# Optimization experiments

Measured on AMD Instinct MI355X. Metric: run time of the kernel, lower is better.

The kernel has to match this reference:

```python
import jax, jax.numpy as jnp
import numpy as np


def _sobel_weights():
    # ImageGradientsLayer: fixed Sobel x/y filters, shape (O=2, I=1, 3, 3)
    gx = jnp.array([[-1., 0., 1.], [-2., 0., 2.], [-1., 0., 1.]], dtype=jnp.float32)
    gy = jnp.array([[-1., -2., -1.], [0., 0., 0.], [1., 2., 1.]], dtype=jnp.float32)
    return jnp.stack([gx, gy])[:, None, :, :]


def _orientation_weights():
    # SIFTOrientationLayer: 8 unit orientation vectors + 2x2 identity, shape (10, 2)
    ratios = jnp.arange(0.125, 2.125, 0.25, dtype=jnp.float32)  # 8 values
    ang = ratios * jnp.pi
    vec = jnp.stack([jnp.cos(ang), jnp.sin(ang)], axis=1)  # (8, 2)
    return jnp.concatenate([vec, jnp.eye(2, dtype=jnp.float32)], axis=0)  # (10, 2)


def setup_inputs() -> dict:
    key = jax.random.key(0)
    x = jax.random.normal(key, (8, 1, 1024, 1024), dtype=jnp.float32)
    return {"x": x, "sobel_w": _sobel_weights(), "orient_w": _orientation_weights()}


def reference(x, sobel_w, orient_w):
    # 1) ImageGradientsLayer: 3x3 Sobel conv, padding=1 -> (B, 2, H, W)
    grads = jax.lax.conv_general_dilated(
        x, sobel_w, window_strides=(1, 1), padding=((1, 1), (1, 1)),
        dimension_numbers=("NCHW", "OIHW", "NCHW"))
    # 2) SIFTOrientationLayer: 1x1 conv == channel projection -> (B, 10, H, W)
    proj = jnp.einsum("bchw,oc->bohw", grads, orient_w)
    # 3) HistogramLayer: one-hot(argmax of orientation dots) * gradient magnitude
    cosines = proj[:, :8]          # (B, 8, H, W)
    im_grads = proj[:, 8:]         # (B, 2, H, W) == grads (identity rows)
    magnitudes = jnp.sqrt(jnp.sum(im_grads * im_grads, axis=1))  # (B, H, W)
    max_idx = jnp.argmax(cosines, axis=1)                        # (B, H, W)
    onehot = jax.nn.one_hot(max_idx, 8, axis=1, dtype=x.dtype)   # (B, 8, H, W)
    hist = onehot * magnitudes[:, None, :, :]
    # 4) SubGridAccumulationLayer: depthwise 4x4 all-ones conv, pad 2 -> (B, 8, H+1, W+1)
    ones_k = jnp.ones((8, 1, 4, 4), dtype=x.dtype)
    out = jax.lax.conv_general_dilated(
        hist, ones_k, window_strides=(1, 1), padding=((2, 2), (2, 2)),
        dimension_numbers=("NCHW", "OIHW", "NCHW"), feature_group_count=8)
    return out
```

## Files before the change

kernel.cpp:

```cpp
#include <hip/hip_runtime.h>
#include <math.h>


#define TWC 61
#define WTH 16
#define WPB 4
#define BTH (WPB*WTH)
#define XC 66
#define XR (BTH+5)
#define PLANE 1050625
#define NCT 17
#define NRT 17

__device__ __forceinline__ float wshl1(float v) {
    return __int_as_float(
        __builtin_amdgcn_update_dpp(0, __float_as_int(v), 0x130, 0xf, 0xf, true));
}

__global__ __launch_bounds__(256, 4)
void sift_fused(const float* __restrict__ x,
                const float* __restrict__ ow,
                float* __restrict__ out)
{
    __shared__ float sx[XR * XC];

    const int tid  = threadIdx.x;
    const int lane = tid & 63;
    const int wv   = tid >> 6;

    const int flat = blockIdx.x + NCT * (blockIdx.y + NRT * blockIdx.z);
    const int bb = flat & 7;
    const int t  = flat >> 3;
    const int bx = t % NCT;
    const int by = t / NCT;
    const int j0 = bx * TWC;
    const int r0 = by * BTH;

    const float* xb = x + (size_t)bb * 1024 * 1024;
    for (int p = tid; p < XR * XC; p += 256) {
        int r = p / XC, c = p - r * XC;
        int gr = r0 - 3 + r, gc = j0 - 3 + c;
        float v = 0.0f;
        if ((unsigned)gr < 1024u && (unsigned)gc < 1024u)
            v = xb[(size_t)gr * 1024 + gc];
        sx[p] = v;
    }
    __syncthreads();

    const int rbase = r0 + WTH * wv;
    if (rbase > 1024) return;

    float wcn[8], wsn[8];
    #pragma unroll
    for (int o = 0; o < 8; ++o) { wcn[o] = ow[2*o]; wsn[o] = ow[2*o+1]; }

    const int gcol = j0 - 2 + lane;
    const bool colok = (unsigned)gcol < 1024u;
    const int gj = j0 + lane;
    const bool canstore = (lane < TWC) && (gj <= 1024);

    float* po[8];
    #pragma unroll
    for (int o = 0; o < 8; ++o) po[o] = out + (size_t)(bb * 8 + o) * PLANE;

    const float* px = sx + (WTH * wv) * XC + lane;
    int hrow = rbase - 2;
    int orow = rbase;
    int vo   = rbase * 1025 + gj;

    float dd0, dd1, dd2, dd3, ww0, ww1, ww2, ww3;
    float cA[8], cB[8], PP0[8], PP1[8], PP2[8], PP3[8];

#define XROWLOAD(DD, WW) { \
    float n0 = px[0], n1 = px[1], n2 = px[2]; px += XC; \
    DD = n2 - n0; \
    WW = n0 + 2.0f*n1 + n2; \
}

#define HSTEP(DT, DM, DB, WT, WB, CP, CC, PR, PC, DOP, DOFIN) { \
    XROWLOAD(DB, WB) \
    float gx = DT + 2.0f*DM + DB; \
    float gy = WB - WT; \
    float msq = gx*gx + gy*gy; \
    float m = (colok && (unsigned)hrow < 1024u) \
                ? __builtin_amdgcn_sqrtf(msq) : 0.0f; \
    hrow++; \
    float pj0 = gx*wcn[0] + gy*wsn[0]; \
    float pj1 = gx*wcn[1] + gy*wsn[1]; \
    float pj2 = gx*wcn[2] + gy*wsn[2]; \
    float pj3 = gx*wcn[3] + gy*wsn[3]; \
    float pj4 = gx*wcn[4] + gy*wsn[4]; \
    float pj5 = gx*wcn[5] + gy*wsn[5]; \
    float pj6 = gx*wcn[6] + gy*wsn[6]; \
    float pj7 = gx*wcn[7] + gy*wsn[7]; \
    bool g01 = pj1 > pj0; float b01 = g01 ? pj1 : pj0; int i01 = g01 ? 1 : 0; \
    bool g23 = pj3 > pj2; float b23 = g23 ? pj3 : pj2; int i23 = g23 ? 3 : 2; \
    bool g45 = pj5 > pj4; float b45 = g45 ? pj5 : pj4; int i45 = g45 ? 5 : 4; \
    bool g67 = pj7 > pj6; float b67 = g67 ? pj7 : pj6; int i67 = g67 ? 7 : 6; \
    bool gA = b23 > b01; float bA = gA ? b23 : b01; int iA = gA ? i23 : i01; \
    bool gB = b67 > b45; float bB = gB ? b67 : b45; int iB = gB ? i67 : i45; \
    int idx = (bB > bA) ? iB : iA; \
    _Pragma("unroll") \
    for (int o = 0; o < 8; ++o) CC[o] = (idx == o) ? m : 0.0f; \
    if (DOP) { \
        _Pragma("unroll") \
        for (int o = 0; o < 8; ++o) PC[o] = CP[o] + CC[o]; \
    } \
    if (DOFIN) { \
        bool ok = canstore && (orow <= 1024); \
        _Pragma("unroll") \
        for (int o = 0; o < 8; ++o) { \
            float v = PR[o] + PC[o]; \
            v += wshl1(v);                  \
            v += wshl1(wshl1(v));           \
            if (ok) po[o][vo] = v; \
        } \
        vo += 1025; orow++; \
    } \
}

    XROWLOAD(dd0, ww0)
    XROWLOAD(dd1, ww1)
    HSTEP(dd0, dd1, dd2, ww0, ww2, cA, cB, PP0, PP0, 0, 0)
    HSTEP(dd1, dd2, dd3, ww1, ww3, cB, cA, PP0, PP1, 1, 0)
    HSTEP(dd2, dd3, dd0, ww2, ww0, cA, cB, PP0, PP2, 1, 0)

    #pragma unroll 1
    for (int it = 0; it < 4; ++it) {
        HSTEP(dd3, dd0, dd1, ww3, ww1, cB, cA, PP1, PP3, 1, 1)
        HSTEP(dd0, dd1, dd2, ww0, ww2, cA, cB, PP2, PP0, 1, 1)
        HSTEP(dd1, dd2, dd3, ww1, ww3, cB, cA, PP3, PP1, 1, 1)
        HSTEP(dd2, dd3, dd0, ww2, ww0, cA, cB, PP0, PP2, 1, 1)
    }

#undef HSTEP
#undef XROWLOAD
}

extern "C" void kernel_launch(void* const* d_in, const int* in_sizes, int n_in,
                              void* d_out, int out_size, void* d_ws, size_t ws_size,
                              hipStream_t stream)
{
    (void)in_sizes; (void)n_in; (void)d_ws; (void)ws_size; (void)out_size;
    const float* x  = (const float*)d_in[0];
    const float* ow = (const float*)d_in[2];
    float* out = (float*)d_out;

    dim3 grid(NCT, NRT, 8);
    sift_fused<<<grid, 256, 0, stream>>>(x, ow, out);
}
```

Baseline: 88.49 us.

## Drop LDS staging; load rows directly with float2, two columns per lane

Replaces the shared-memory tile load and block barrier with per-lane direct global float2 loads of each input row, prefetched one row ahead in registers. Each lane now computes two output columns, using DPP lane shifts for the horizontal neighbours. Blocks become 9-wave column strips over 33-row bands. This is meant to remove LDS traffic, the sync, and halo overhead per output, at the cost of higher register pressure and unaligned or redundant global loads.

```diff
diff --git a/kernel.cpp b/kernel.cpp
--- a/kernel.cpp
+++ b/kernel.cpp
@@ -2,139 +2,165 @@
 #include <math.h>
 
 
-#define TWC 61
-#define WTH 16
-#define WPB 4
-#define BTH (WPB*WTH)
-#define XC 66
-#define XR (BTH+5)
+#define BROWS 33
+#define NBANDS 32
+#define STRIPW 124
 #define PLANE 1050625
-#define NCT 17
-#define NRT 17
 
 __device__ __forceinline__ float wshl1(float v) {
     return __int_as_float(
         __builtin_amdgcn_update_dpp(0, __float_as_int(v), 0x130, 0xf, 0xf, true));
 }
 
-__global__ __launch_bounds__(256, 4)
+__global__ __launch_bounds__(576, 3)
 void sift_fused(const float* __restrict__ x,
                 const float* __restrict__ ow,
                 float* __restrict__ out)
 {
-    __shared__ float sx[XR * XC];
-
     const int tid  = threadIdx.x;
     const int lane = tid & 63;
     const int wv   = tid >> 6;
 
-    const int flat = blockIdx.x + NCT * (blockIdx.y + NRT * blockIdx.z);
-    const int bb = flat & 7;
-    const int t  = flat >> 3;
-    const int bx = t % NCT;
-    const int by = t / NCT;
-    const int j0 = bx * TWC;
-    const int r0 = by * BTH;
+    const int flat = blockIdx.x + NBANDS * blockIdx.y;
+    const int bb   = flat & 7;
+    const int band = flat >> 3;
+    const int r0 = band * BROWS;
+    const int j0 = wv * STRIPW;
 
     const float* xb = x + (size_t)bb * 1024 * 1024;
-    for (int p = tid; p < XR * XC; p += 256) {
-        int r = p / XC, c = p - r * XC;
-        int gr = r0 - 3 + r, gc = j0 - 3 + c;
-        float v = 0.0f;
-        if ((unsigned)gr < 1024u && (unsigned)gc < 1024u)
-            v = xb[(size_t)gr * 1024 + gc];
-        sx[p] = v;
-    }
-    __syncthreads();
-
-    const int rbase = r0 + WTH * wv;
-    if (rbase > 1024) return;
 
     float wcn[8], wsn[8];
     #pragma unroll
     for (int o = 0; o < 8; ++o) { wcn[o] = ow[2*o]; wsn[o] = ow[2*o+1]; }
 
-    const int gcol = j0 - 2 + lane;
-    const bool colok = (unsigned)gcol < 1024u;
-    const int gj = j0 + lane;
-    const bool canstore = (lane < TWC) && (gj <= 1024);
+    const int c1 = j0 - 4 + 2*lane;
+    const int s1 = min(max(c1,     0), 1022);
+    const int s2 = min(max(c1 + 2, 0), 1022);
+    const float mB = ((unsigned)(c1+1) < 1024u) ? 1.f : 0.f;
+    const float mC = ((unsigned)(c1+2) < 1024u) ? 1.f : 0.f;
+    const float mD = ((unsigned)(c1+3) < 1024u) ? 1.f : 0.f;
+
+    const int h0 = j0 - 2 + 2*lane;
+    const float cm0 = ((unsigned)h0     < 1024u) ? 1.f : 0.f;
+    const float cm1 = ((unsigned)(h0+1) < 1024u) ? 1.f : 0.f;
+
+    const int oc0 = j0 + 2*lane;
+    const bool st0 = (2*lane   < STRIPW) && (oc0   <= 1024);
+    const bool st1 = (2*lane+1 < STRIPW) && (oc0+1 <= 1024);
 
     float* po[8];
     #pragma unroll
-    for (int o = 0; o < 8; ++o) po[o] = out + (size_t)(bb * 8 + o) * PLANE;
+    for (int o = 0; o < 8; ++o) po[o] = out + (size_t)(bb*8 + o) * PLANE;
 
-    const float* px = sx + (WTH * wv) * XC + lane;
-    int hrow = rbase - 2;
-    int orow = rbase;
-    int vo   = rbase * 1025 + gj;
+    int vo   = r0 * 1025 + oc0;
+    int orow = r0;
+    int gr   = r0 - 3;
+    int hrow = r0 - 2;
 
-    float dd0, dd1, dd2, dd3, ww0, ww1, ww2, ww3;
-    float cA[8], cB[8], PP0[8], PP1[8], PP2[8], PP3[8];
+    float RD[4][2], RW[4][2];
+    float CEXP[2][2][8];
+    float PP[4][2][8];
+    float2 pv1, pv2;
 
-#define XROWLOAD(DD, WW) { \
-    float n0 = px[0], n1 = px[1], n2 = px[2]; px += XC; \
-    DD = n2 - n0; \
-    WW = n0 + 2.0f*n1 + n2; \
+#define XISSUE() { \
+    if ((unsigned)gr < 1024u) { \
+        const float* rp = xb + ((size_t)(unsigned)gr << 10); \
+        pv1 = *reinterpret_cast<const float2*>(rp + s1); \
+        pv2 = *reinterpret_cast<const float2*>(rp + s2); \
+    } else { pv1.x = 0.f; pv1.y = 0.f; pv2.x = 0.f; pv2.y = 0.f; } \
+    gr++; \
 }
 
-#define HSTEP(DT, DM, DB, WT, WB, CP, CC, PR, PC, DOP, DOFIN) { \
-    XROWLOAD(DB, WB) \
-    float gx = DT + 2.0f*DM + DB; \
-    float gy = WB - WT; \
-    float msq = gx*gx + gy*gy; \
-    float m = (colok && (unsigned)hrow < 1024u) \
-                ? __builtin_amdgcn_sqrtf(msq) : 0.0f; \
-    hrow++; \
-    float pj0 = gx*wcn[0] + gy*wsn[0]; \
-    float pj1 = gx*wcn[1] + gy*wsn[1]; \
-    float pj2 = gx*wcn[2] + gy*wsn[2]; \
-    float pj3 = gx*wcn[3] + gy*wsn[3]; \
-    float pj4 = gx*wcn[4] + gy*wsn[4]; \
-    float pj5 = gx*wcn[5] + gy*wsn[5]; \
-    float pj6 = gx*wcn[6] + gy*wsn[6]; \
-    float pj7 = gx*wcn[7] + gy*wsn[7]; \
+#define XCOMMIT(SB) { \
+    float B_ = pv1.y * mB, C_ = pv2.x * mC, D_ = pv2.y * mD; \
+    float E_ = wshl1(C_); \
+    RD[SB][0] = D_ - B_; \
+    RD[SB][1] = E_ - C_; \
+    RW[SB][0] = B_ + 2.0f*C_ + D_; \
+    RW[SB][1] = C_ + 2.0f*D_ + E_; \
+}
+
+#define TOURN8(RES, GX, GY) { \
+    float pj0 = (GX)*wcn[0] + (GY)*wsn[0]; \
+    float pj1 = (GX)*wcn[1] + (GY)*wsn[1]; \
+    float pj2 = (GX)*wcn[2] + (GY)*wsn[2]; \
+    float pj3 = (GX)*wcn[3] + (GY)*wsn[3]; \
+    float pj4 = (GX)*wcn[4] + (GY)*wsn[4]; \
+    float pj5 = (GX)*wcn[5] + (GY)*wsn[5]; \
+    float pj6 = (GX)*wcn[6] + (GY)*wsn[6]; \
+    float pj7 = (GX)*wcn[7] + (GY)*wsn[7]; \
     bool g01 = pj1 > pj0; float b01 = g01 ? pj1 : pj0; int i01 = g01 ? 1 : 0; \
     bool g23 = pj3 > pj2; float b23 = g23 ? pj3 : pj2; int i23 = g23 ? 3 : 2; \
     bool g45 = pj5 > pj4; float b45 = g45 ? pj5 : pj4; int i45 = g45 ? 5 : 4; \
     bool g67 = pj7 > pj6; float b67 = g67 ? pj7 : pj6; int i67 = g67 ? 7 : 6; \
     bool gA = b23 > b01; float bA = gA ? b23 : b01; int iA = gA ? i23 : i01; \
     bool gB = b67 > b45; float bB = gB ? b67 : b45; int iB = gB ? i67 : i45; \
-    int idx = (bB > bA) ? iB : iA; \
+    RES = (bB > bA) ? iB : iA; \
+}
+
+#define HSTEP(ST, SM, SB, EC, EP, PW, PRD, DOP, DOFIN) { \
+    XCOMMIT(SB) \
+    XISSUE() \
+    float rowm = ((unsigned)hrow < 1024u) ? 1.f : 0.f; \
+    hrow++; \
     _Pragma("unroll") \
-    for (int o = 0; o < 8; ++o) CC[o] = (idx == o) ? m : 0.0f; \
+    for (int c_ = 0; c_ < 2; ++c_) { \
+        float gx = RD[ST][c_] + 2.0f*RD[SM][c_] + RD[SB][c_]; \
+        float gy = RW[SB][c_] - RW[ST][c_]; \
+        float m = __builtin_amdgcn_sqrtf(gx*gx + gy*gy) \
+                    * (rowm * (c_ ? cm1 : cm0)); \
+        int idx_; \
+        TOURN8(idx_, gx, gy) \
+        _Pragma("unroll") \
+        for (int o = 0; o < 8; ++o) \
+            CEXP[EC][c_][o] = (idx_ == o) ? m : 0.0f; \
+    } \
     if (DOP) { \
         _Pragma("unroll") \
-        for (int o = 0; o < 8; ++o) PC[o] = CP[o] + CC[o]; \
+        for (int c_ = 0; c_ < 2; ++c_) { \
+            _Pragma("unroll") \
+            for (int o = 0; o < 8; ++o) \
+                PP[PW][c_][o] = CEXP[EP][c_][o] + CEXP[EC][c_][o]; \
+        } \
     } \
     if (DOFIN) { \
-        bool ok = canstore && (orow <= 1024); \
+        bool rowok = (orow <= 1024); \
         _Pragma("unroll") \
         for (int o = 0; o < 8; ++o) { \
-            float v = PR[o] + PC[o]; \
-            v += wshl1(v);                  \
-            v += wshl1(wshl1(v));           \
-            if (ok) po[o][vo] = v; \
+            float A  = PP[PRD][0][o] + PP[PW][0][o]; \
+            float Bv = PP[PRD][1][o] + PP[PW][1][o]; \
+            float S  = A + Bv; \
+            float Sd = wshl1(S); \
+            float Ad2 = wshl1(wshl1(A)); \
+            float Ev = S + Sd; \
+            float Ov = Bv + Sd + Ad2; \
+            if (rowok && st0) po[o][vo]   = Ev; \
+            if (rowok && st1) po[o][vo+1] = Ov; \
         } \
         vo += 1025; orow++; \
     } \
 }
 
-    XROWLOAD(dd0, ww0)
-    XROWLOAD(dd1, ww1)
-    HSTEP(dd0, dd1, dd2, ww0, ww2, cA, cB, PP0, PP0, 0, 0)
-    HSTEP(dd1, dd2, dd3, ww1, ww3, cB, cA, PP0, PP1, 1, 0)
-    HSTEP(dd2, dd3, dd0, ww2, ww0, cA, cB, PP0, PP2, 1, 0)
+    XISSUE()
+    XCOMMIT(0) XISSUE()
+    XCOMMIT(1) XISSUE()
+    HSTEP(0,1,2, 0,1, 0,0, 0, 0)
+    HSTEP(1,2,3, 1,0, 1,3, 1, 0)
+    HSTEP(2,3,0, 0,1, 2,0, 1, 0)
 
     #pragma unroll 1
-    for (int it = 0; it < 4; ++it) {
-        HSTEP(dd3, dd0, dd1, ww3, ww1, cB, cA, PP1, PP3, 1, 1)
-        HSTEP(dd0, dd1, dd2, ww0, ww2, cA, cB, PP2, PP0, 1, 1)
-        HSTEP(dd1, dd2, dd3, ww1, ww3, cB, cA, PP3, PP1, 1, 1)
-        HSTEP(dd2, dd3, dd0, ww2, ww0, cA, cB, PP0, PP2, 1, 1)
+    for (int it = 0; it < 8; ++it) {
+        HSTEP(3,0,1, 1,0, 3,1, 1, 1)
+        HSTEP(0,1,2, 0,1, 0,2, 1, 1)
+        HSTEP(1,2,3, 1,0, 1,3, 1, 1)
+        HSTEP(2,3,0, 0,1, 2,0, 1, 1)
     }
+    HSTEP(3,0,1, 1,0, 3,1, 1, 1)
 
 #undef HSTEP
-#undef XROWLOAD
+#undef TOURN8
+#undef XCOMMIT
+#undef XISSUE
 }
 
 extern "C" void kernel_launch(void* const* d_in, const int* in_sizes, int n_in,
@@ -146,6 +172,6 @@
     const float* ow = (const float*)d_in[2];
     float* out = (float*)d_out;
 
-    dim3 grid(NCT, NRT, 8);
-    sift_fused<<<grid, 256, 0, stream>>>(x, ow, out);
+    dim3 grid(NBANDS, 8, 1);
+    sift_fused<<<grid, 576, 0, stream>>>(x, ow, out);
 }
```

Result: slower. 119.4 us (+34.9%).
